# Kernel tuning notes

Hardware: AMD Instinct MI355X
Metric: run time of the kernel (lower is better)

Reference implementation:

```python
import jax, jax.numpy as jnp
import numpy as np

B, T, C, H = 4, 2048, 1024, 16
D = C // H  # head_size = 64


def setup_inputs() -> dict:
    key = jax.random.key(0)
    k1, k2, k3 = jax.random.split(key, 3)
    h = jax.random.normal(k1, (B, T, C), dtype=jnp.float32)
    # additive float mask, [B,1,1,T]; zeros = no padding
    attention_mask = jnp.zeros((B, 1, 1, T), dtype=jnp.float32)
    # learned params (bias=False linears), scaled like default torch init
    w_attn = jax.random.normal(k2, (C, 3 * C), dtype=jnp.float32) / np.sqrt(C)
    w_proj = jax.random.normal(k3, (C, C), dtype=jnp.float32) / np.sqrt(C)
    return {"h": h, "attention_mask": attention_mask, "w_attn": w_attn, "w_proj": w_proj}


def reference(h, attention_mask, w_attn, w_proj):
    # fused QKV projection: [B,T,3C]
    qkv = jnp.einsum("btc,cd->btd", h, w_attn)
    q, k, v = jnp.split(qkv, 3, axis=-1)
    # [B,T,C] -> [B,H,T,D]
    def to_heads(x):
        return x.reshape(B, T, H, D).transpose(0, 2, 1, 3)
    q, k, v = to_heads(q), to_heads(k), to_heads(v)
    # scaled dot-product attention with additive mask (non-causal)
    scale = 1.0 / np.sqrt(D).astype(np.float32)
    scores = jnp.einsum("bhqd,bhkd->bhqk", q, k) * scale + attention_mask
    probs = jax.nn.softmax(scores, axis=-1)
    y = jnp.einsum("bhqk,bhkd->bhqd", probs, v)
    # [B,H,T,D] -> [B,T,C]
    y = y.transpose(0, 2, 1, 3).reshape(B, T, C)
    return jnp.einsum("btc,cd->btd", y, w_proj)
```

## Files before the change

kernel.cpp:

```cpp
#include <hip/hip_runtime.h>
#include <hip/hip_bf16.h>

#define DEV static __device__ __forceinline__

typedef __attribute__((ext_vector_type(4))) float f32x4;
typedef __attribute__((ext_vector_type(16))) float f32x16;
typedef __attribute__((ext_vector_type(8))) short bf16x8;

constexpr int Bb = 4, Ts = 2048, Cc = 1024, Hh = 16, Dd = 64;
constexpr int Mm = Bb * Ts;
constexpr float SCQ = 0.18033688f;

union frag_u {
  bf16x8 f;
  uint2  u2[2];
  ushort us[8];
  uint4  u4;
};

DEV ushort f2bf(float x) {
  union { float f; unsigned u; } v; v.f = x;
  unsigned r = v.u + 0x7FFFu + ((v.u >> 16) & 1u);
  return (ushort)(r >> 16);
}

DEV ushort f2bf_hw(float x) {
  union { __hip_bfloat16 b; ushort u; } cv;
  cv.b = __float2bfloat16(x);
  return cv.u;
}

typedef const __attribute__((address_space(1))) unsigned int gu32;
typedef __attribute__((address_space(3))) unsigned int lu32;
DEV void gload16(const void* g, void* l) {
  __builtin_amdgcn_global_load_lds((gu32*)g, (lu32*)l, 16, 0, 0);
}

DEV void ld_frag16(frag_u& fr, const ushort* lds, int row, int chunk) {
  int off = row * 128 + ((chunk ^ (row & 7)) << 4);
  fr.u4 = *reinterpret_cast<const uint4*>(reinterpret_cast<const char*>(lds) + off);
}
DEV void ld_frag16w(frag_u& fr, const ushort* lds, int row, int chunk) {
  int off = row * 256 + ((chunk ^ (row & 15)) << 4);
  fr.u4 = *reinterpret_cast<const uint4*>(reinterpret_cast<const char*>(lds) + off);
}
DEV void vst64w(ushort* lds, int row, int col, uint2 v) {
  int off = row * 256 + ((((col >> 3) ^ (row & 15)) << 4) | ((2 * col) & 15));
  *reinterpret_cast<uint2*>(reinterpret_cast<char*>(lds) + off) = v;
}

DEV void eW64b(char* E, int row, int col, uint2 v) {
  int off = row * 256 + ((((col >> 3) ^ (row & 15)) << 4) | ((col & 7) * 2));
  *reinterpret_cast<uint2*>(E + off) = v;
}
DEV uint4 eR128b(const char* E, int row, int dc) {
  int off = row * 256 + ((dc ^ (row & 15)) << 4);
  return *reinterpret_cast<const uint4*>(E + off);
}

__global__ __launch_bounds__(256) void cvt_kernel(const float* __restrict__ in,
                                                  ushort* __restrict__ out, int n4) {
  for (int i = blockIdx.x * blockDim.x + threadIdx.x; i < n4;
       i += gridDim.x * blockDim.x) {
    float4 v = reinterpret_cast<const float4*>(in)[i];
    ushort4 o;
    o.x = f2bf(v.x); o.y = f2bf(v.y); o.z = f2bf(v.z); o.w = f2bf(v.w);
    reinterpret_cast<ushort4*>(out)[i] = o;
  }
}

__global__ __launch_bounds__(256) void expmask_kernel(const float* __restrict__ m,
                                                      float* __restrict__ em, int n) {
  int i = blockIdx.x * blockDim.x + threadIdx.x;
  if (i < n) em[i] = __expf(m[i]);
}

__global__ __launch_bounds__(256) void transpose_cvt(const float* __restrict__ in,
                                                     ushort* __restrict__ out,
                                                     int R, int Ccols) {
  __shared__ float tile[32][33];
  int c0 = blockIdx.x * 32, r0 = blockIdx.y * 32;
  int tx = threadIdx.x & 31, ty = threadIdx.x >> 5;
#pragma unroll
  for (int i = 0; i < 4; ++i) {
    int r = ty + i * 8;
    tile[r][tx] = in[(size_t)(r0 + r) * Ccols + c0 + tx];
  }
  __syncthreads();
#pragma unroll
  for (int i = 0; i < 4; ++i) {
    int r = ty + i * 8;
    out[(size_t)(c0 + r) * R + r0 + tx] = f2bf(tile[tx][r]);
  }
}

template <int EPI>
__global__ __launch_bounds__(256) void gemm_bt(const ushort* __restrict__ A,
                                               const ushort* __restrict__ Bt,
                                               int M, int N, int K,
                                               float* __restrict__ Cf,
                                               ushort* __restrict__ Qb,
                                               ushort* __restrict__ Kb,
                                               ushort* __restrict__ Vb,
                                               const float* __restrict__ expm) {
  __shared__ ushort Lds[2][128 * 64];
  __shared__ float evals[128];
  ushort* Al = Lds[0];
  ushort* Bl = Lds[1];
  const int tid = threadIdx.x;
  const int lane = tid & 63, wid = tid >> 6;
  const int l31 = lane & 31, lh = lane >> 5;
  const int wr = wid >> 1, wc = wid & 1;
  const int m0 = blockIdx.y * 128, n0 = blockIdx.x * 128;

  if (EPI == 1 && tid < 128)
    evals[tid] = expm[(size_t)(m0 >> 11) * Ts + (m0 & 2047) + tid];

  f32x16 acc[2][2];
#pragma unroll
  for (int mi = 0; mi < 2; ++mi)
#pragma unroll
    for (int nj = 0; nj < 2; ++nj)
#pragma unroll
      for (int r = 0; r < 16; ++r) acc[mi][nj][r] = 0.f;

  const int nkt = K >> 6;
  for (int kt = 0; kt < nkt; ++kt) {
#pragma unroll
    for (int it = 0; it < 4; ++it) {
      int chunk = wid * 256 + it * 64 + lane;
      int row = chunk >> 3, c16 = (chunk & 7) ^ (row & 7);
      gload16(A + (size_t)(m0 + row) * K + kt * 64 + c16 * 8,
              Al + (size_t)(wid * 256 + it * 64) * 8);
      gload16(Bt + (size_t)(n0 + row) * K + kt * 64 + c16 * 8,
              Bl + (size_t)(wid * 256 + it * 64) * 8);
    }
    __syncthreads();
#pragma unroll
    for (int kk = 0; kk < 4; ++kk) {
      const int chunk = kk * 2 + lh;
      frag_u af[2], bfr[2];
#pragma unroll
      for (int mi = 0; mi < 2; ++mi)
        ld_frag16(af[mi], Al, wr * 64 + mi * 32 + l31, chunk);
#pragma unroll
      for (int nj = 0; nj < 2; ++nj)
        ld_frag16(bfr[nj], Bl, wc * 64 + nj * 32 + l31, chunk);
#pragma unroll
      for (int mi = 0; mi < 2; ++mi)
#pragma unroll
        for (int nj = 0; nj < 2; ++nj)
          acc[mi][nj] = __builtin_amdgcn_mfma_f32_32x32x16_bf16(
              af[mi].f, bfr[nj].f, acc[mi][nj], 0, 0, 0);
    }
    __syncthreads();
  }

  if (EPI == 0) {
#pragma unroll
    for (int mi = 0; mi < 2; ++mi)
#pragma unroll
      for (int nj = 0; nj < 2; ++nj) {
        int ncol = n0 + wc * 64 + nj * 32 + l31;
#pragma unroll
        for (int r = 0; r < 16; ++r) {
          int mrow = m0 + wr * 64 + mi * 32 + (r & 3) + 8 * (r >> 2) + 4 * lh;
          Cf[(size_t)mrow * N + ncol] = acc[mi][nj][r];
        }
      }
  } else {
    const int seg = n0 >> 10;
    const int hd0 = (n0 & 1023) >> 6;
    const int bq = m0 >> 11, tt0 = m0 & 2047;
    if (seg < 2) {
      const float vs = (seg == 0) ? SCQ : 1.0f;
      ushort* dstQ = (seg == 0) ? Qb : Kb;
#pragma unroll
      for (int mi = 0; mi < 2; ++mi)
#pragma unroll
        for (int nj = 0; nj < 2; ++nj) {
          int colb = wc * 64 + nj * 32 + l31;
          int hd = hd0 + (colb >> 6), d = colb & 63;
          ushort* gb = dstQ + (size_t)(bq * Hh + hd) * Ts * Dd + d;
#pragma unroll
          for (int r = 0; r < 16; ++r) {
            int tt = tt0 + wr * 64 + mi * 32 + (r & 3) + 8 * (r >> 2) + 4 * lh;
            gb[(size_t)tt * Dd] = f2bf(acc[mi][nj][r] * vs);
          }
        }
    } else {
      char* E = reinterpret_cast<char*>(&Lds[0][0]);
#pragma unroll
      for (int mi = 0; mi < 2; ++mi)
#pragma unroll
        for (int nj = 0; nj < 2; ++nj) {
          int erow = wc * 64 + nj * 32 + l31;
#pragma unroll
          for (int q2 = 0; q2 < 4; ++q2) {
            int tb = wr * 64 + mi * 32 + 8 * q2 + 4 * lh;
            float e0 = evals[tb], e1 = evals[tb + 1];
            float e2 = evals[tb + 2], e3 = evals[tb + 3];
            unsigned lo = (unsigned)f2bf(acc[mi][nj][4 * q2 + 0] * e0) |
                          ((unsigned)f2bf(acc[mi][nj][4 * q2 + 1] * e1) << 16);
            unsigned hi = (unsigned)f2bf(acc[mi][nj][4 * q2 + 2] * e2) |
                          ((unsigned)f2bf(acc[mi][nj][4 * q2 + 3] * e3) << 16);
            eW64b(E, erow, tb, uint2{lo, hi});
          }
        }
      __syncthreads();
#pragma unroll
      for (int k = 0; k < 8; ++k) {
        int c = k * 256 + tid;
        int row = c >> 4, t16 = c & 15;
        int hd = hd0 + (row >> 6), d = row & 63;
        uint4 v = eR128b(E, row, t16);
        *reinterpret_cast<uint4*>(
            Vb + ((size_t)(bq * Hh + hd) * Dd + d) * Ts + tt0 + t16 * 8) = v;
      }
    }
  }
}

__global__ __launch_bounds__(512, 4) void attn_kernel(const ushort* __restrict__ Qb,
                                                      const ushort* __restrict__ Kb,
                                                      const ushort* __restrict__ VTb,
                                                      const float* __restrict__ expm,
                                                      ushort* __restrict__ Yb) {
  __shared__ ushort Klds[2][128 * 64];
  __shared__ ushort Vlds[2][64 * 128];
  __shared__ ushort wlds[2][128];

  const int tid = threadIdx.x;
  const int lane = tid & 63, wid = tid >> 6;
  const int g = lane >> 4, l15 = lane & 15;
  const int bh = blockIdx.x;
  const int b = bh >> 4, h = bh & 15;
  const int qt = blockIdx.y;

  const ushort* Qh = Qb + (size_t)bh * Ts * Dd;
  const ushort* Kh = Kb + (size_t)bh * Ts * Dd;
  const ushort* Vh = VTb + (size_t)bh * Dd * Ts;
  const float* erow = expm + (size_t)b * Ts;

  const int kch0 = wid * 64 + lane, kch1 = kch0 + 512;
  const int kr0 = kch0 >> 3, kc0 = (kch0 & 7) ^ (kr0 & 7);
  const int kr1 = kch1 >> 3, kc1 = (kch1 & 7) ^ (kr1 & 7);
  const int vrow0 = tid >> 4, vc16 = tid & 15;
  const int vrow1 = vrow0 + 32;
  const int vkh = vc16 >> 3, vc8 = vc16 & 7;
  const int vcol = vkh * 64 + 32 * (vc8 >> 2) + 16 * (vc8 & 1) + 4 * ((vc8 >> 1) & 1);
  const int t6 = tid & 63;
  const int wp = (tid & 64) | (t6 & 32) | ((t6 & 12) << 1) | ((t6 & 16) >> 2) | (t6 & 3);

  frag_u aq[2][2];
#pragma unroll
  for (int qsub = 0; qsub < 2; ++qsub) {
    const ushort* qp = Qh + (size_t)(qt * 256 + wid * 32 + qsub * 16 + l15) * Dd;
#pragma unroll
    for (int ks = 0; ks < 2; ++ks)
      aq[qsub][ks].u4 = *reinterpret_cast<const uint4*>(qp + ks * 32 + 8 * g);
  }

  f32x4 acc[2][4];
  f32x4 lacc[2];
#pragma unroll
  for (int q = 0; q < 2; ++q) {
    lacc[q] = f32x4{0.f, 0.f, 0.f, 0.f};
#pragma unroll
    for (int dt = 0; dt < 4; ++dt) acc[q][dt] = f32x4{0.f, 0.f, 0.f, 0.f};
  }

  uint4 vreg0, vreg1;
  float wreg = 0.f;

#define ISSUE(kt, buf)                                                          \
  gload16(Kh + (size_t)((kt) * 128 + kr0) * Dd + kc0 * 8,                       \
          Klds[buf] + (size_t)(wid * 64) * 8);                                  \
  gload16(Kh + (size_t)((kt) * 128 + kr1) * Dd + kc1 * 8,                       \
          Klds[buf] + (size_t)(512 + wid * 64) * 8);                            \
  vreg0 = *reinterpret_cast<const uint4*>(Vh + (size_t)vrow0 * Ts + (kt) * 128 + vc16 * 8); \
  vreg1 = *reinterpret_cast<const uint4*>(Vh + (size_t)vrow1 * Ts + (kt) * 128 + vc16 * 8); \
  wreg = (tid < 128) ? erow[(kt) * 128 + tid] : 0.f;

#define COMMIT(buf)                                                             \
  vst64w(Vlds[buf], vrow0, vcol, uint2{vreg0.x, vreg0.y});                      \
  vst64w(Vlds[buf], vrow0, vcol + 8, uint2{vreg0.z, vreg0.w});                  \
  vst64w(Vlds[buf], vrow1, vcol, uint2{vreg1.x, vreg1.y});                      \
  vst64w(Vlds[buf], vrow1, vcol + 8, uint2{vreg1.z, vreg1.w});                  \
  if (tid < 128) wlds[buf][wp] = f2bf_hw(wreg);

  ISSUE(0, 0);
  COMMIT(0);
  __syncthreads();

  const int NT = Ts / 128;
  for (int kt = 0; kt < NT; ++kt) {
    const int cur = kt & 1;
    const bool more = (kt + 1 < NT);
    if (more) { ISSUE(kt + 1, cur ^ 1); }

#pragma unroll
    for (int kh = 0; kh < 2; ++kh) {
      f32x4 s[2][4];
#pragma unroll
      for (int q = 0; q < 2; ++q)
#pragma unroll
        for (int n = 0; n < 4; ++n) s[q][n] = f32x4{0.f, 0.f, 0.f, 0.f};
      __builtin_amdgcn_s_setprio(1);
#pragma unroll
      for (int ks = 0; ks < 2; ++ks)
#pragma unroll
        for (int n = 0; n < 4; ++n) {
          frag_u bk;
          ld_frag16(bk, Klds[cur], kh * 64 + n * 16 + l15, 4 * ks + g);
#pragma unroll
          for (int q = 0; q < 2; ++q)
            s[q][n] = __builtin_amdgcn_mfma_f32_16x16x32_bf16(bk.f, aq[q][ks].f,
                                                              s[q][n], 0, 0, 0);
        }
      __builtin_amdgcn_s_setprio(0);

      frag_u pa[2][2];
#pragma unroll
      for (int q = 0; q < 2; ++q)
#pragma unroll
        for (int n = 0; n < 4; ++n)
#pragma unroll
          for (int r = 0; r < 4; ++r)
            pa[q][n >> 1].us[(n & 1) * 4 + r] =
                f2bf_hw(__builtin_amdgcn_exp2f(s[q][n][r]));

      frag_u wf[2];
      wf[0].u4 = *reinterpret_cast<const uint4*>(&wlds[cur][kh * 64 + 8 * g]);
      wf[1].u4 = *reinterpret_cast<const uint4*>(&wlds[cur][kh * 64 + 32 + 8 * g]);
      __builtin_amdgcn_s_setprio(1);
#pragma unroll
      for (int ks = 0; ks < 2; ++ks)
#pragma unroll
        for (int q = 0; q < 2; ++q)
          lacc[q] = __builtin_amdgcn_mfma_f32_16x16x32_bf16(pa[q][ks].f, wf[ks].f,
                                                            lacc[q], 0, 0, 0);
#pragma unroll
      for (int ks = 0; ks < 2; ++ks)
#pragma unroll
        for (int dt = 0; dt < 4; ++dt) {
          frag_u bv;
          ld_frag16w(bv, Vlds[cur], dt * 16 + l15, kh * 8 + 4 * ks + g);
#pragma unroll
          for (int q = 0; q < 2; ++q)
            acc[q][dt] = __builtin_amdgcn_mfma_f32_16x16x32_bf16(pa[q][ks].f, bv.f,
                                                                 acc[q][dt], 0, 0, 0);
        }
      __builtin_amdgcn_s_setprio(0);
    }

    if (more) { COMMIT(cur ^ 1); }
    __syncthreads();
  }
#undef ISSUE
#undef COMMIT

#pragma unroll
  for (int q = 0; q < 2; ++q) {
#pragma unroll
    for (int r = 0; r < 4; ++r) {
      float inv = 1.0f / lacc[q][r];
      int t = qt * 256 + wid * 32 + q * 16 + 4 * g + r;
      size_t base = ((size_t)(b * Ts + t)) * Cc + h * Dd;
#pragma unroll
      for (int dt = 0; dt < 4; ++dt)
        Yb[base + dt * 16 + l15] = f2bf(acc[q][dt][r] * inv);
    }
  }
}

extern "C" void kernel_launch(void* const* d_in, const int* in_sizes, int n_in,
                              void* d_out, int out_size, void* d_ws, size_t ws_size,
                              hipStream_t stream) {
  const float* h    = (const float*)d_in[0];
  const float* mask = (const float*)d_in[1];
  const float* wa   = (const float*)d_in[2];
  const float* wp   = (const float*)d_in[3];
  float* out = (float*)d_out;

  char* ws = (char*)d_ws;
  ushort* hbf     = (ushort*)(ws);
  ushort* wattn_t = (ushort*)(ws + (16u << 20));
  ushort* wproj_t = (ushort*)(ws + (22u << 20));
  ushort* Qb      = (ushort*)(ws + (24u << 20));
  ushort* Kb      = (ushort*)(ws + (40u << 20));
  ushort* VTb     = (ushort*)(ws + (56u << 20));
  float*  expm    = (float*)(ws + (72u << 20));
  ushort* Ybf = hbf;

  cvt_kernel<<<2048, 256, 0, stream>>>(h, hbf, (Mm * Cc) / 4);
  expmask_kernel<<<(Bb * Ts + 255) / 256, 256, 0, stream>>>(mask, expm, Bb * Ts);
  transpose_cvt<<<dim3(3 * Cc / 32, Cc / 32), 256, 0, stream>>>(wa, wattn_t, Cc, 3 * Cc);
  transpose_cvt<<<dim3(Cc / 32, Cc / 32), 256, 0, stream>>>(wp, wproj_t, Cc, Cc);

  gemm_bt<1><<<dim3(3 * Cc / 128, Mm / 128), 256, 0, stream>>>(
      hbf, wattn_t, Mm, 3 * Cc, Cc, nullptr, Qb, Kb, VTb, expm);

  attn_kernel<<<dim3(Bb * Hh, Ts / 256), 512, 0, stream>>>(Qb, Kb, VTb, expm, Ybf);

  gemm_bt<0><<<dim3(Cc / 128, Mm / 128), 256, 0, stream>>>(
      Ybf, wproj_t, Mm, Cc, Cc, out, nullptr, nullptr, nullptr, nullptr);
}
```

Baseline: 170.6 us.

## Double-buffer GEMM LDS tiles to overlap global loads with MFMA

```diff
diff --git a/kernel.cpp b/kernel.cpp
--- a/kernel.cpp
+++ b/kernel.cpp
@@ -103,10 +103,9 @@
                                                ushort* __restrict__ Kb,
                                                ushort* __restrict__ Vb,
                                                const float* __restrict__ expm) {
-  __shared__ ushort Lds[2][128 * 64];
+  __shared__ ushort Al[2][128 * 64];
+  __shared__ ushort Bl[2][128 * 64];
   __shared__ float evals[128];
-  ushort* Al = Lds[0];
-  ushort* Bl = Lds[1];
   const int tid = threadIdx.x;
   const int lane = tid & 63, wid = tid >> 6;
   const int l31 = lane & 31, lh = lane >> 5;
@@ -116,6 +115,18 @@
   if (EPI == 1 && tid < 128)
     evals[tid] = expm[(size_t)(m0 >> 11) * Ts + (m0 & 2047) + tid];
 
+#define ISSUE(slot, t)                                                          \
+  {                                                                             \
+    _Pragma("unroll") for (int it = 0; it < 4; ++it) {                          \
+      int chunk = wid * 256 + it * 64 + lane;                                   \
+      int row = chunk >> 3, c16 = (chunk & 7) ^ (row & 7);                      \
+      gload16(A + (size_t)(m0 + row) * K + (t) * 64 + c16 * 8,                  \
+              Al[slot] + (size_t)(wid * 256 + it * 64) * 8);                    \
+      gload16(Bt + (size_t)(n0 + row) * K + (t) * 64 + c16 * 8,                 \
+              Bl[slot] + (size_t)(wid * 256 + it * 64) * 8);                    \
+    }                                                                           \
+  }
+
   f32x16 acc[2][2];
 #pragma unroll
   for (int mi = 0; mi < 2; ++mi)
@@ -125,27 +136,23 @@
       for (int r = 0; r < 16; ++r) acc[mi][nj][r] = 0.f;
 
   const int nkt = K >> 6;
+  ISSUE(0, 0);
   for (int kt = 0; kt < nkt; ++kt) {
-#pragma unroll
-    for (int it = 0; it < 4; ++it) {
-      int chunk = wid * 256 + it * 64 + lane;
-      int row = chunk >> 3, c16 = (chunk & 7) ^ (row & 7);
-      gload16(A + (size_t)(m0 + row) * K + kt * 64 + c16 * 8,
-              Al + (size_t)(wid * 256 + it * 64) * 8);
-      gload16(Bt + (size_t)(n0 + row) * K + kt * 64 + c16 * 8,
-              Bl + (size_t)(wid * 256 + it * 64) * 8);
-    }
-    __syncthreads();
+    const int s = kt & 1;
+    const int tn = (kt + 1 < nkt) ? kt + 1 : nkt - 1;
+    ISSUE(s ^ 1, tn);
+    asm volatile("s_waitcnt vmcnt(8)" ::: "memory");
+    __builtin_amdgcn_s_barrier();
 #pragma unroll
     for (int kk = 0; kk < 4; ++kk) {
       const int chunk = kk * 2 + lh;
       frag_u af[2], bfr[2];
 #pragma unroll
       for (int mi = 0; mi < 2; ++mi)
-        ld_frag16(af[mi], Al, wr * 64 + mi * 32 + l31, chunk);
+        ld_frag16(af[mi], Al[s], wr * 64 + mi * 32 + l31, chunk);
 #pragma unroll
       for (int nj = 0; nj < 2; ++nj)
-        ld_frag16(bfr[nj], Bl, wc * 64 + nj * 32 + l31, chunk);
+        ld_frag16(bfr[nj], Bl[s], wc * 64 + nj * 32 + l31, chunk);
 #pragma unroll
       for (int mi = 0; mi < 2; ++mi)
 #pragma unroll
@@ -153,8 +160,11 @@
           acc[mi][nj] = __builtin_amdgcn_mfma_f32_32x32x16_bf16(
               af[mi].f, bfr[nj].f, acc[mi][nj], 0, 0, 0);
     }
-    __syncthreads();
-  }
+    __builtin_amdgcn_s_barrier();
+  }
+#undef ISSUE
+  asm volatile("s_waitcnt vmcnt(0)" ::: "memory");
+  __syncthreads();
 
   if (EPI == 0) {
 #pragma unroll
@@ -189,7 +199,7 @@
           }
         }
     } else {
-      char* E = reinterpret_cast<char*>(&Lds[0][0]);
+      char* E = reinterpret_cast<char*>(&Al[0][0]);
 #pragma unroll
       for (int mi = 0; mi < 2; ++mi)
 #pragma unroll
```

Result: slower. 176.9 us (+3.7%).
